# Optimization experiments

Hardware: AMD Instinct MI355X
Metric: run time of the kernel (lower is better)

The kernel has to match this reference:

```python
import jax, jax.numpy as jnp
import numpy as np

EPS = 1e-6
DIM_HEAD = 32
INP = 128
OUP = 128
IH = IW = 32


def _conv3x3(x, w):
    # NCHW conv, 3x3, stride 1, pad 1, no bias
    return jax.lax.conv_general_dilated(
        x, w, window_strides=(1, 1), padding=((1, 1), (1, 1)),
        dimension_numbers=("NCHW", "OIHW", "NCHW"))


def _groupnorm1(x, gamma, beta):
    # GroupNorm with 1 group: normalize over (C,H,W) per sample
    m = jnp.mean(x, axis=(1, 2, 3), keepdims=True)
    v = jnp.var(x, axis=(1, 2, 3), keepdims=True)
    xn = (x - m) * jax.lax.rsqrt(v + EPS)
    return xn * gamma[None, :, None, None] + beta[None, :, None, None]


def _proj(x, w, gamma, beta):
    return jax.nn.gelu(_groupnorm1(_conv3x3(x, w), gamma, beta), approximate=False)


def _relative_index(ih, iw):
    coords = np.stack(np.meshgrid(np.arange(ih), np.arange(iw), indexing="ij"))
    coords = coords.reshape(2, -1)  # (2, N)
    rel = coords[:, :, None] - coords[:, None, :]  # (2, N, N)
    rel[0] += ih - 1
    rel[1] += iw - 1
    rel[0] *= 2 * iw - 1
    return rel.sum(0).reshape(-1).astype(np.int32)  # (N*N,)


def setup_inputs() -> dict:
    key = jax.random.key(0)
    ks = jax.random.split(key, 12)
    B = 16
    x = jax.random.normal(ks[0], (B, INP, IH, IW), jnp.float32)
    w_scale = 0.05
    wq = jax.random.normal(ks[1], (INP, INP, 3, 3), jnp.float32) * w_scale
    wk = jax.random.normal(ks[2], (INP, INP, 3, 3), jnp.float32) * w_scale
    wv = jax.random.normal(ks[3], (INP, INP, 3, 3), jnp.float32) * w_scale
    gq = jnp.ones((INP,), jnp.float32); bq = jnp.zeros((INP,), jnp.float32)
    gk = jnp.ones((INP,), jnp.float32); bk = jnp.zeros((INP,), jnp.float32)
    gv = jnp.ones((INP,), jnp.float32); bv = jnp.zeros((INP,), jnp.float32)
    heads = INP // DIM_HEAD
    table = jax.random.normal(ks[4], ((2 * IH - 1) * (2 * IW - 1), heads), jnp.float32) * 0.02
    rel_index = jnp.asarray(_relative_index(IH, IW))
    out_w = jax.random.normal(ks[5], (OUP, INP, 1, 1), jnp.float32) * w_scale
    out_b = jnp.zeros((OUP,), jnp.float32)
    return {"x": x, "wq": wq, "gq": gq, "bq": bq, "wk": wk, "gk": gk, "bk": bk,
            "wv": wv, "gv": gv, "bv": bv, "table": table, "rel_index": rel_index,
            "out_w": out_w, "out_b": out_b}


def reference(x, wq, gq, bq, wk, gk, bk, wv, gv, bv, table, rel_index, out_w, out_b):
    B, C, ih, iw = x.shape
    H = C // DIM_HEAD
    N = ih * iw

    def to_heads(t):
        # b c ih iw -> b (ihiw) c -> b h n d (heads-major channel split)
        return t.reshape(B, C, N).transpose(0, 2, 1).reshape(B, N, H, DIM_HEAD).transpose(0, 2, 1, 3)

    q = to_heads(_proj(x, wq, gq, bq))
    k = to_heads(_proj(x, wk, gk, bk))
    v = to_heads(_proj(x, wv, gv, bv))

    # NOTE: original applies self.scale only when y is not None; y=None here -> no scale
    dots = jnp.einsum("bhnd,bhmd->bhnm", q, k)  # (B,H,N,N)

    bias = table[rel_index]                 # (N*N, H)
    bias = bias.reshape(N, N, H).transpose(2, 0, 1)[None]  # (1,H,N,N)
    attn = jax.nn.softmax(dots + bias, axis=-1)

    out = jnp.einsum("bhnm,bhmd->bhnd", attn, v)
    out = out.transpose(0, 2, 1, 3).reshape(B, N, C).transpose(0, 2, 1).reshape(B, C, ih, iw)
    # to_out: 1x1 conv + bias (Dropout2d is identity in eval)
    out = jax.lax.conv_general_dilated(
        out, out_w, window_strides=(1, 1), padding=((0, 0), (0, 0)),
        dimension_numbers=("NCHW", "OIHW", "NCHW")) + out_b[None, :, None, None]
    return out
```

## Files before the change

### kernel.cpp

```cpp
#include <hip/hip_runtime.h>

typedef unsigned short u16;
typedef unsigned int   u32;

#define NB   16
#define NC   128
#define NPIX 1024
#define NH   4
#define DH   32

typedef __attribute__((ext_vector_type(8))) short short8;
typedef __attribute__((ext_vector_type(4))) float f32x4;
typedef __attribute__((ext_vector_type(8))) _Float16 half8;

#define XROWS 1152

__device__ __forceinline__ float bf2f(u16 u) {
    return __uint_as_float(((u32)u) << 16);
}
__device__ __forceinline__ u16 f2bf(float f) {
    u32 u = __float_as_uint(f);
    u32 r = (u + 0x7fffu + ((u >> 16) & 1u)) >> 16;
    return (u16)r;
}
__device__ __forceinline__ u16 f2h(float f) {
    _Float16 h = (_Float16)f;
    u16 r; __builtin_memcpy(&r, &h, 2); return r;
}
__device__ __forceinline__ int pk_h2(float a, float b) {
    auto h = __builtin_amdgcn_cvt_pkrtz(a, b);
    int r; __builtin_memcpy(&r, &h, 4); return r;
}
__device__ __forceinline__ float loadf(const void* p, int i, int isf) {
    return isf ? ((const float*)p)[i] : bf2f(((const u16*)p)[i]);
}
__device__ __forceinline__ float4 load4(const void* p, int i4, int isf) {
    if (isf) return ((const float4*)p)[i4];
    ushort4 u = ((const ushort4*)p)[i4];
    return make_float4(bf2f(u.x), bf2f(u.y), bf2f(u.z), bf2f(u.w));
}
__device__ __forceinline__ int detect_isf(const void* x) {
    const u16* p = (const u16*)x;
    u16 v = p[threadIdx.x & 63];
    int e = (v >> 7) & 0xFF;
    unsigned long long m = __ballot(e >= 134);
    return m != 0ull ? 1 : 0;
}

__global__ __launch_bounds__(256) void prep_all(
        const void* __restrict__ x,
        const void* __restrict__ w0, const void* __restrict__ w1,
        const void* __restrict__ w2, const void* __restrict__ ow,
        const int* __restrict__ rel, const void* __restrict__ table,
        u16* __restrict__ Wt, u16* __restrict__ Wf, u16* __restrict__ xTp,
        u16* __restrict__ biasT, float* __restrict__ stats) {
    __shared__ __align__(16) u32 smem_u[4160];
    int isf = detect_isf(x);
    int bid = blockIdx.x;
    int t = threadIdx.x;

    if (bid < 1792) {
        if (bid == 0 && t < 96) stats[t] = 0.f;
        int i = bid * 256 + t;
        if (i < 442368) {
            int j   = i / 147456;
            int rr  = i % 147456;
            int tap = rr >> 14;
            int co  = (rr >> 7) & 127;
            int ci  = rr & 127;
            const void* w = (j == 0) ? w0 : ((j == 1) ? w1 : w2);
            float v = loadf(w, (co * 128 + ci) * 9 + tap, isf);
            Wt[i] = f2bf(v);
        } else {
            int i2 = i - 442368;
            if (i2 < 16384) Wf[i2] = f2h(loadf(ow, i2, isf));
        }
    } else if (bid < 2304) {
        float* tile = (float*)smem_u;
        int b2 = bid - 1792;
        int pixg = b2 & 7, cig = (b2 >> 3) & 3, b = b2 >> 5;

        if (pixg == 0 || pixg == 7) {
            int row = (pixg == 0 ? 0 : 1088) + (t >> 2);
            int seg = t & 3;
            size_t dst = ((size_t)(b * XROWS + row)) * 128 + cig * 32 + seg * 8;
            *(uint4*)&xTp[dst] = make_uint4(0, 0, 0, 0);
        }

        int ci = t >> 3, px0 = (t & 7) * 16;
        int base = b * (NC * NPIX) + (cig * 32 + ci) * NPIX + pixg * 128 + px0;
#pragma unroll
        for (int u = 0; u < 4; ++u) {
            float4 v = load4(x, (base >> 2) + u, isf);
            float* d = &tile[ci * 129 + px0 + u * 4];
            d[0] = v.x; d[1] = v.y; d[2] = v.z; d[3] = v.w;
        }
        __syncthreads();
#pragma unroll
        for (int u = 0; u < 2; ++u) {
            int c = t + u * 256;
            int pix = c >> 2, seg = c & 3;
            u16 tmp[8];
#pragma unroll
            for (int e = 0; e < 8; ++e)
                tmp[e] = f2bf(tile[(seg * 8 + e) * 129 + pix]);
            size_t dst = ((size_t)(b * XROWS + 64 + pixg * 128 + pix)) * 128
                       + cig * 32 + seg * 8;
            *(ushort4*)&xTp[dst] =
                make_ushort4(tmp[0], tmp[1], tmp[2], tmp[3]);
            *(ushort4*)&xTp[dst + 4] =
                make_ushort4(tmp[4], tmp[5], tmp[6], tmp[7]);
        }
    } else {
        int* rl = (int*)smem_u;
        int b2 = bid - 2304;
        int nt = b2 & 15, mt = b2 >> 4;

#pragma unroll
        for (int c = 0; c < 16; ++c) {
            int i = t + c * 256;
            int r = i >> 6, cc = i & 63;
            rl[r * 65 + cc] = rel[(size_t)(nt * 64 + r) * 1024 + mt * 64 + cc];
        }
        __syncthreads();

#pragma unroll
        for (int h = 0; h < NH; ++h) {
#pragma unroll
            for (int c = 0; c < 16; ++c) {
                int wdx = t + c * 256;
                int m = wdx >> 6, n = wdx & 63;
                int ri = rl[n * 65 + m];
                float v = loadf(table, ri * NH + h, isf);
                biasT[((size_t)h << 20) + (size_t)(mt * 64 + m) * 1024
                      + nt * 64 + n] = f2bf(v);
            }
        }
    }
}

__global__ __launch_bounds__(256) void conv6_kernel(
        const u16* __restrict__ xTp, const u16* __restrict__ Wt,
        float* __restrict__ conv_out, float* __restrict__ stats) {
    __shared__ __align__(16) u16 Xh[194 * 128];

    int t = threadIdx.x;
    int pt = blockIdx.x, b = blockIdx.y, j = blockIdx.z;
    int p0 = pt * 128;
    int w = t >> 6, lane = t & 63;
    int q = lane >> 4, l16 = lane & 15;
    int cobase = (w & 1) * 64;
    int pixbase = (w >> 1) * 64;

    const u16* xb  = xTp + ((size_t)b * XROWS + 64) * 128;
    const u16* wjb = Wt + (size_t)j * 9 * 16384;

#pragma unroll
    for (int k = 0; k < 13; ++k) {
        int c = t + k * 256;
        if (c < 194 * 16) {
            int row = c >> 4, seg = c & 15;
            int pg = p0 - 33 + row;
            uint4 v = *(const uint4*)(xb + (size_t)pg * 128 + seg * 8);
            *(uint4*)&Xh[row * 128 + ((seg + row) & 15) * 8] = v;
        }
    }
    __syncthreads();

    f32x4 acc[4][4];
#pragma unroll
    for (int mt = 0; mt < 4; ++mt)
#pragma unroll
        for (int nt = 0; nt < 4; ++nt) acc[mt][nt] = (f32x4)0.f;

    for (int tap = 0; tap < 9; ++tap) {
        int dy = tap / 3, dx = tap % 3;
        bool inv_e = (dx == 0) && (l16 == 0);
        bool inv_o = (dx == 2) && (l16 == 15);
        int rbase = pixbase + dy * 32 + dx + l16;
        const u16* wt = wjb + tap * 16384;
#pragma unroll
        for (int ks = 0; ks < 4; ++ks) {
            int k0 = ks * 32 + q * 8;
            int sl = ks * 4 + q;
            short8 a[4], bf[4];
#pragma unroll
            for (int mt = 0; mt < 4; ++mt)
                a[mt] = *(const short8*)(wt
                        + (size_t)(cobase + mt * 16 + l16) * 128 + k0);
#pragma unroll
            for (int nt = 0; nt < 4; ++nt) {
                int row = rbase + nt * 16;
                short8 v = *(const short8*)&Xh[row * 128
                                               + ((sl + row) & 15) * 8];
                bf[nt] = ((nt & 1) ? inv_o : inv_e) ? (short8)0 : v;
            }
#pragma unroll
            for (int mt = 0; mt < 4; ++mt)
#pragma unroll
                for (int nt = 0; nt < 4; ++nt)
                    acc[mt][nt] = __builtin_amdgcn_mfma_f32_16x16x32_bf16(
                        a[mt], bf[nt], acc[mt][nt], 0, 0, 0);
        }
    }

    float s = 0.f, s2 = 0.f;
    size_t obase = ((size_t)(j * NB + b) * NC) * NPIX;
#pragma unroll
    for (int mt = 0; mt < 4; ++mt) {
#pragma unroll
        for (int nt = 0; nt < 4; ++nt) {
            f32x4 v = acc[mt][nt];
            int co  = cobase + mt * 16 + q * 4;
            int pix = p0 + pixbase + nt * 16 + l16;
#pragma unroll
            for (int r = 0; r < 4; ++r) {
                float val = v[r];
                conv_out[obase + (size_t)(co + r) * NPIX + pix] = val;
                s += val;
                s2 = fmaf(val, val, s2);
            }
        }
    }
#pragma unroll
    for (int off = 32; off; off >>= 1) {
        s  += __shfl_down(s,  (unsigned)off, 64);
        s2 += __shfl_down(s2, (unsigned)off, 64);
    }
    if (lane == 0) {
        atomicAdd(&stats[(j * NB + b) * 2 + 0], s);
        atomicAdd(&stats[(j * NB + b) * 2 + 1], s2);
    }
}

__global__ __launch_bounds__(256) void norm_kernel(
        const void* __restrict__ xdet,
        const float* __restrict__ conv_out, const float* __restrict__ stats,
        const void* __restrict__ g0, const void* __restrict__ b0,
        const void* __restrict__ g1, const void* __restrict__ b1,
        const void* __restrict__ g2, const void* __restrict__ b2,
        u16* __restrict__ qh, u16* __restrict__ kh, u16* __restrict__ vh) {
    __shared__ float tile[32 * 257];
    int isf = detect_isf(xdet);
    int t = threadIdx.x;
    int n0 = blockIdx.x * 256;
    int h = blockIdx.y;
    int z = blockIdx.z;
    int j = z >> 4;
    int b = z & 15;
    const void* gam = (j == 0) ? g0 : ((j == 1) ? g1 : g2);
    const void* bet = (j == 0) ? b0 : ((j == 1) ? b1 : b2);

    float sum = stats[z * 2], ss = stats[z * 2 + 1];
    const float inv = 1.0f / 131072.0f;
    float mean = sum * inv;
    float var  = fmaxf(ss * inv - mean * mean, 0.f);
    float rstd = rsqrtf(var + 1e-6f);

    const float* src = conv_out + ((size_t)z * NC + h * DH) * NPIX + n0;

    if (j == 2) {
        u16* dst = vh + (((size_t)(b * NH + h)) * DH) * NPIX + n0;
#pragma unroll
        for (int cl = 0; cl < 32; ++cl) {
            float v = src[cl * NPIX + t];
            v = (v - mean) * rstd * loadf(gam, h * DH + cl, isf)
              + loadf(bet, h * DH + cl, isf);
            v = 0.5f * v * (1.0f + erff(v * 0.70710678118654752f));
            dst[(size_t)cl * NPIX + t] = f2h(v);
        }
        return;
    }

#pragma unroll
    for (int cl = 0; cl < 32; ++cl) tile[cl * 257 + t] = src[cl * NPIX + t];
    __syncthreads();

    u16* dst = ((j == 0) ? qh : kh)
             + (((size_t)(b * NH + h)) * NPIX + n0) * DH;
#pragma unroll
    for (int k = 0; k < 32; ++k) {
        int o = t + k * 256;
        int d = o & 31, nl = o >> 5;
        float v = tile[d * 257 + nl];
        v = (v - mean) * rstd * loadf(gam, h * DH + d, isf)
          + loadf(bet, h * DH + d, isf);
        v = 0.5f * v * (1.0f + erff(v * 0.70710678118654752f));
        dst[o] = f2h(v);
    }
}

__global__ __launch_bounds__(256) void attn2_kernel(
        const u16* __restrict__ qh, const u16* __restrict__ kh,
        const u16* __restrict__ vh, const u16* __restrict__ biasT,
        u16* __restrict__ attfh) {
    int t = threadIdx.x;
    int b = blockIdx.x, h = blockIdx.y, qt = blockIdx.z;
    int w = t >> 6, lane = t & 63, q = lane >> 4, l16 = lane & 15;
    int nrow0 = qt * 128 + w * 32;

    const u16* qb = qh + (((size_t)(b * NH + h)) * NPIX) * DH;
    const u16* kb = kh + (((size_t)(b * NH + h)) * NPIX) * DH;
    const u16* vb = vh + (((size_t)(b * NH + h)) * DH) * NPIX;
    const u16* bb = biasT + ((size_t)h << 20);

    half8 qf[2];
#pragma unroll
    for (int nt = 0; nt < 2; ++nt)
        qf[nt] = *(const half8*)(qb + (size_t)(nrow0 + nt * 16 + l16) * DH
                                 + q * 8);

    f32x4 O[2][2];
#pragma unroll
    for (int dt = 0; dt < 2; ++dt)
#pragma unroll
        for (int nt = 0; nt < 2; ++nt) O[dt][nt] = (f32x4)0.f;
    float mrow[2] = {-1e30f, -1e30f}, lrow[2] = {0.f, 0.f};

    int addrLo = ((2 * (q & 1)) * 16 + l16) * 4;
    int addrHi = addrLo + 64;
    bool hiQ = (q >= 2);

    for (int kc = 0; kc < 8; ++kc) {
        int m0 = kc * 128;
        f32x4 St[8][2];
#pragma unroll
        for (int mt = 0; mt < 8; ++mt) {
            half8 kf = *(const half8*)(kb + (size_t)(m0 + mt * 16 + l16) * DH
                                       + q * 8);
            St[mt][0] = __builtin_amdgcn_mfma_f32_16x16x32_f16(
                kf, qf[0], (f32x4)0.f, 0, 0, 0);
            St[mt][1] = __builtin_amdgcn_mfma_f32_16x16x32_f16(
                kf, qf[1], (f32x4)0.f, 0, 0, 0);
        }
        float mx[2] = {-1e30f, -1e30f};
#pragma unroll
        for (int mt = 0; mt < 8; ++mt)
#pragma unroll
            for (int nt = 0; nt < 2; ++nt) {
                const u16* bp = bb + (size_t)(m0 + mt * 16 + q * 4) * 1024
                              + nrow0 + nt * 16 + l16;
#pragma unroll
                for (int r = 0; r < 4; ++r) {
                    float v = St[mt][nt][r] + bf2f(bp[(size_t)r * 1024]);
                    St[mt][nt][r] = v;
                    mx[nt] = fmaxf(mx[nt], v);
                }
            }
        float alpha[2];
#pragma unroll
        for (int nt = 0; nt < 2; ++nt) {
            mx[nt] = fmaxf(mx[nt], __shfl_xor(mx[nt], 16, 64));
            mx[nt] = fmaxf(mx[nt], __shfl_xor(mx[nt], 32, 64));
            float mn = fmaxf(mrow[nt], mx[nt]);
            alpha[nt] = __expf(mrow[nt] - mn);
            mrow[nt] = mn;
        }
        float sm[2] = {0.f, 0.f};
#pragma unroll
        for (int mt = 0; mt < 8; ++mt)
#pragma unroll
            for (int nt = 0; nt < 2; ++nt)
#pragma unroll
                for (int r = 0; r < 4; ++r) {
                    float p = __expf(St[mt][nt][r] - mrow[nt]);
                    St[mt][nt][r] = p;
                    sm[nt] += p;
                }
#pragma unroll
        for (int nt = 0; nt < 2; ++nt) {
            sm[nt] += __shfl_xor(sm[nt], 16, 64);
            sm[nt] += __shfl_xor(sm[nt], 32, 64);
            lrow[nt] = lrow[nt] * alpha[nt] + sm[nt];
        }
#pragma unroll
        for (int dt = 0; dt < 2; ++dt)
#pragma unroll
            for (int nt = 0; nt < 2; ++nt)
#pragma unroll
                for (int r = 0; r < 4; ++r)
                    O[dt][nt][r] *= alpha[nt];
#pragma unroll
        for (int ms = 0; ms < 4; ++ms) {
            half8 vf[2];
#pragma unroll
            for (int dt = 0; dt < 2; ++dt)
                vf[dt] = *(const half8*)(vb + (size_t)(dt * 16 + l16) * NPIX
                                         + m0 + ms * 32 + q * 8);
#pragma unroll
            for (int nt = 0; nt < 2; ++nt) {
                int p01_0 = pk_h2(St[2 * ms][nt][0],     St[2 * ms][nt][1]);
                int p23_0 = pk_h2(St[2 * ms][nt][2],     St[2 * ms][nt][3]);
                int p01_1 = pk_h2(St[2 * ms + 1][nt][0], St[2 * ms + 1][nt][1]);
                int p23_1 = pk_h2(St[2 * ms + 1][nt][2], St[2 * ms + 1][nt][3]);
                int a0 = __builtin_amdgcn_ds_bpermute(addrLo, p01_0);
                int a1 = __builtin_amdgcn_ds_bpermute(addrLo, p23_0);
                int a2 = __builtin_amdgcn_ds_bpermute(addrHi, p01_0);
                int a3 = __builtin_amdgcn_ds_bpermute(addrHi, p23_0);
                int b0 = __builtin_amdgcn_ds_bpermute(addrLo, p01_1);
                int b1 = __builtin_amdgcn_ds_bpermute(addrLo, p23_1);
                int b2 = __builtin_amdgcn_ds_bpermute(addrHi, p01_1);
                int b3 = __builtin_amdgcn_ds_bpermute(addrHi, p23_1);
                int pb[4];
                pb[0] = hiQ ? b0 : a0;
                pb[1] = hiQ ? b1 : a1;
                pb[2] = hiQ ? b2 : a2;
                pb[3] = hiQ ? b3 : a3;
                half8 pf; __builtin_memcpy(&pf, pb, 16);
#pragma unroll
                for (int dt = 0; dt < 2; ++dt)
                    O[dt][nt] = __builtin_amdgcn_mfma_f32_16x16x32_f16(
                        vf[dt], pf, O[dt][nt], 0, 0, 0);
            }
        }
    }

#pragma unroll
    for (int nt = 0; nt < 2; ++nt) {
        float rl = 1.0f / lrow[nt];
        int n = nrow0 + nt * 16 + l16;
        u16* dst = attfh + ((size_t)b * NPIX + n) * NC + h * DH;
#pragma unroll
        for (int dt = 0; dt < 2; ++dt) {
            f32x4 o = O[dt][nt];
            uint2 pv = make_uint2((u32)pk_h2(o[0] * rl, o[1] * rl),
                                  (u32)pk_h2(o[2] * rl, o[3] * rl));
            *(uint2*)(dst + dt * 16 + q * 4) = pv;
        }
    }
}

__global__ __launch_bounds__(256) void out3_kernel(
        const void* __restrict__ xdet,
        const u16* __restrict__ attfh, const u16* __restrict__ Wf,
        const void* __restrict__ ob, void* __restrict__ out) {
    int isf = detect_isf(xdet);
    int t = threadIdx.x;
    int n0 = blockIdx.x * 64, b = blockIdx.y;
    int w = t >> 6, lane = t & 63, q = lane >> 4, l16 = lane & 15;
    int cobase = (w & 1) * 64, nbase = (w >> 1) * 32;

    f32x4 acc[4][2];
#pragma unroll
    for (int mt = 0; mt < 4; ++mt)
#pragma unroll
        for (int nt = 0; nt < 2; ++nt) acc[mt][nt] = (f32x4)0.f;

    const u16* ab = attfh + ((size_t)b * NPIX + n0 + nbase) * NC;
#pragma unroll
    for (int ks = 0; ks < 4; ++ks) {
        int k0 = ks * 32 + q * 8;
        half8 a[4], bfr[2];
#pragma unroll
        for (int mt = 0; mt < 4; ++mt)
            a[mt] = *(const half8*)(Wf + (size_t)(cobase + mt * 16 + l16) * NC
                                    + k0);
#pragma unroll
        for (int nt = 0; nt < 2; ++nt)
            bfr[nt] = *(const half8*)(ab + (size_t)(nt * 16 + l16) * NC + k0);
#pragma unroll
        for (int mt = 0; mt < 4; ++mt)
#pragma unroll
            for (int nt = 0; nt < 2; ++nt)
                acc[mt][nt] = __builtin_amdgcn_mfma_f32_16x16x32_f16(
                    a[mt], bfr[nt], acc[mt][nt], 0, 0, 0);
    }

#pragma unroll
    for (int mt = 0; mt < 4; ++mt) {
#pragma unroll
        for (int nt = 0; nt < 2; ++nt) {
            f32x4 v = acc[mt][nt];
            int n = n0 + nbase + nt * 16 + l16;
#pragma unroll
            for (int r = 0; r < 4; ++r) {
                int co = cobase + mt * 16 + q * 4 + r;
                float val = v[r] + loadf(ob, co, isf);
                size_t oidx = ((size_t)b * NC + co) * NPIX + n;
                if (isf) ((float*)out)[oidx] = val;
                else     ((u16*)out)[oidx]   = f2bf(val);
            }
        }
    }
}

extern "C" void kernel_launch(void* const* d_in, const int* in_sizes, int n_in,
                              void* d_out, int out_size, void* d_ws,
                              size_t ws_size, hipStream_t stream) {
    (void)in_sizes; (void)n_in; (void)out_size; (void)ws_size;
    const void* x     = d_in[0];
    const void* wq    = d_in[1];
    const void* gq    = d_in[2];
    const void* bq    = d_in[3];
    const void* wk    = d_in[4];
    const void* gk    = d_in[5];
    const void* bk    = d_in[6];
    const void* wv    = d_in[7];
    const void* gv    = d_in[8];
    const void* bv    = d_in[9];
    const void* table = d_in[10];
    const int*  rel   = (const int*)d_in[11];
    const void* ow    = d_in[12];
    const void* ob    = d_in[13];

    char* ws = (char*)d_ws;
    float* stats = (float*)(ws);
    char*  regQ  = ws + 512;
    u16*   xTp   = (u16*)regQ;
    u16*   Wt    = (u16*)(regQ + 5242880);
    u16*   qhp   = (u16*)regQ;
    u16*   khp   = (u16*)(regQ + 4194304);
    u16*   vhp   = (u16*)(regQ + 8388608);
    u16*   biasT = (u16*)(regQ + 12582912);
    u16*   Wf    = (u16*)(regQ + 20971520);
    char*  regA  = regQ + 25165824;
    float* conv  = (float*)regA;
    u16*   attfh = (u16*)(regA + 8388608);

    prep_all<<<2560, 256, 0, stream>>>(x, wq, wk, wv, ow, rel, table,
                                       Wt, Wf, xTp, biasT, stats);
    conv6_kernel<<<dim3(8, 16, 3), 256, 0, stream>>>(xTp, Wt, conv, stats);
    norm_kernel<<<dim3(4, 4, 48), 256, 0, stream>>>(x, conv, stats,
                                                    gq, bq, gk, bk, gv, bv,
                                                    qhp, khp, vhp);
    attn2_kernel<<<dim3(16, 4, 8), 256, 0, stream>>>(qhp, khp, vhp, biasT,
                                                     attfh);
    out3_kernel<<<dim3(16, 16), 256, 0, stream>>>(x, attfh, Wf, ob, d_out);
}
```

Baseline: 213.9 us.

## Store bias row-major for vector loads; halve conv pixel tile for more blocks

The relative-position bias is now written in natural (n,m) order straight from rel_index, with no shared-memory transpose. The attention kernel then reads four consecutive bias values with one 8-byte load instead of four strided scalar loads. The conv kernel's pixel tile drops from 128 to 64 per block, doubling the grid from 384 to 768 blocks for better occupancy and lowering LDS use. The cost is more redundant weight loads and more halo rows per block.

```diff
diff --git a/kernel.cpp b/kernel.cpp
--- a/kernel.cpp
+++ b/kernel.cpp
@@ -53,7 +53,7 @@
         const void* __restrict__ w2, const void* __restrict__ ow,
         const int* __restrict__ rel, const void* __restrict__ table,
         u16* __restrict__ Wt, u16* __restrict__ Wf, u16* __restrict__ xTp,
-        u16* __restrict__ biasT, float* __restrict__ stats) {
+        u16* __restrict__ biasb, float* __restrict__ stats) {
     __shared__ __align__(16) u32 smem_u[4160];
     int isf = detect_isf(x);
     int bid = blockIdx.x;
@@ -112,53 +112,42 @@
                 make_ushort4(tmp[4], tmp[5], tmp[6], tmp[7]);
         }
     } else {
-        int* rl = (int*)smem_u;
         int b2 = bid - 2304;
         int nt = b2 & 15, mt = b2 >> 4;
-
 #pragma unroll
         for (int c = 0; c < 16; ++c) {
             int i = t + c * 256;
-            int r = i >> 6, cc = i & 63;
-            rl[r * 65 + cc] = rel[(size_t)(nt * 64 + r) * 1024 + mt * 64 + cc];
-        }
-        __syncthreads();
-
-#pragma unroll
-        for (int h = 0; h < NH; ++h) {
-#pragma unroll
-            for (int c = 0; c < 16; ++c) {
-                int wdx = t + c * 256;
-                int m = wdx >> 6, n = wdx & 63;
-                int ri = rl[n * 65 + m];
-                float v = loadf(table, ri * NH + h, isf);
-                biasT[((size_t)h << 20) + (size_t)(mt * 64 + m) * 1024
-                      + nt * 64 + n] = f2bf(v);
-            }
-        }
-    }
-}
-
-__global__ __launch_bounds__(256) void conv6_kernel(
+            int n = i >> 6, m = i & 63;
+            size_t nm = (size_t)(nt * 64 + n) * 1024 + mt * 64 + m;
+            int ri = rel[nm];
+#pragma unroll
+            for (int h = 0; h < NH; ++h)
+                biasb[((size_t)h << 20) + nm] =
+                    f2bf(loadf(table, ri * NH + h, isf));
+        }
+    }
+}
+
+__global__ __launch_bounds__(256) void conv8_kernel(
         const u16* __restrict__ xTp, const u16* __restrict__ Wt,
         float* __restrict__ conv_out, float* __restrict__ stats) {
-    __shared__ __align__(16) u16 Xh[194 * 128];
+    __shared__ __align__(16) u16 Xh[130 * 128];
 
     int t = threadIdx.x;
     int pt = blockIdx.x, b = blockIdx.y, j = blockIdx.z;
-    int p0 = pt * 128;
+    int p0 = pt * 64;
     int w = t >> 6, lane = t & 63;
     int q = lane >> 4, l16 = lane & 15;
     int cobase = (w & 1) * 64;
-    int pixbase = (w >> 1) * 64;
+    int pixbase = (w >> 1) * 32;
 
     const u16* xb  = xTp + ((size_t)b * XROWS + 64) * 128;
     const u16* wjb = Wt + (size_t)j * 9 * 16384;
 
 #pragma unroll
-    for (int k = 0; k < 13; ++k) {
+    for (int k = 0; k < 9; ++k) {
         int c = t + k * 256;
-        if (c < 194 * 16) {
+        if (c < 130 * 16) {
             int row = c >> 4, seg = c & 15;
             int pg = p0 - 33 + row;
             uint4 v = *(const uint4*)(xb + (size_t)pg * 128 + seg * 8);
@@ -167,11 +156,11 @@
     }
     __syncthreads();
 
-    f32x4 acc[4][4];
+    f32x4 acc[4][2];
 #pragma unroll
     for (int mt = 0; mt < 4; ++mt)
 #pragma unroll
-        for (int nt = 0; nt < 4; ++nt) acc[mt][nt] = (f32x4)0.f;
+        for (int nt = 0; nt < 2; ++nt) acc[mt][nt] = (f32x4)0.f;
 
     for (int tap = 0; tap < 9; ++tap) {
         int dy = tap / 3, dx = tap % 3;
@@ -183,22 +172,22 @@
         for (int ks = 0; ks < 4; ++ks) {
             int k0 = ks * 32 + q * 8;
             int sl = ks * 4 + q;
-            short8 a[4], bf[4];
+            short8 a[4], bf[2];
 #pragma unroll
             for (int mt = 0; mt < 4; ++mt)
                 a[mt] = *(const short8*)(wt
                         + (size_t)(cobase + mt * 16 + l16) * 128 + k0);
 #pragma unroll
-            for (int nt = 0; nt < 4; ++nt) {
+            for (int nt = 0; nt < 2; ++nt) {
                 int row = rbase + nt * 16;
                 short8 v = *(const short8*)&Xh[row * 128
                                                + ((sl + row) & 15) * 8];
-                bf[nt] = ((nt & 1) ? inv_o : inv_e) ? (short8)0 : v;
+                bf[nt] = (nt ? inv_o : inv_e) ? (short8)0 : v;
             }
 #pragma unroll
             for (int mt = 0; mt < 4; ++mt)
 #pragma unroll
-                for (int nt = 0; nt < 4; ++nt)
+                for (int nt = 0; nt < 2; ++nt)
                     acc[mt][nt] = __builtin_amdgcn_mfma_f32_16x16x32_bf16(
                         a[mt], bf[nt], acc[mt][nt], 0, 0, 0);
         }
@@ -209,7 +198,7 @@
 #pragma unroll
     for (int mt = 0; mt < 4; ++mt) {
 #pragma unroll
-        for (int nt = 0; nt < 4; ++nt) {
+        for (int nt = 0; nt < 2; ++nt) {
             f32x4 v = acc[mt][nt];
             int co  = cobase + mt * 16 + q * 4;
             int pix = p0 + pixbase + nt * 16 + l16;
@@ -292,7 +281,7 @@
 
 __global__ __launch_bounds__(256) void attn2_kernel(
         const u16* __restrict__ qh, const u16* __restrict__ kh,
-        const u16* __restrict__ vh, const u16* __restrict__ biasT,
+        const u16* __restrict__ vh, const u16* __restrict__ biasb,
         u16* __restrict__ attfh) {
     int t = threadIdx.x;
     int b = blockIdx.x, h = blockIdx.y, qt = blockIdx.z;
@@ -302,7 +291,7 @@
     const u16* qb = qh + (((size_t)(b * NH + h)) * NPIX) * DH;
     const u16* kb = kh + (((size_t)(b * NH + h)) * NPIX) * DH;
     const u16* vb = vh + (((size_t)(b * NH + h)) * DH) * NPIX;
-    const u16* bb = biasT + ((size_t)h << 20);
+    const u16* bb = biasb + ((size_t)h << 20);
 
     half8 qf[2];
 #pragma unroll
@@ -338,11 +327,13 @@
         for (int mt = 0; mt < 8; ++mt)
 #pragma unroll
             for (int nt = 0; nt < 2; ++nt) {
-                const u16* bp = bb + (size_t)(m0 + mt * 16 + q * 4) * 1024
-                              + nrow0 + nt * 16 + l16;
+                ushort4 u = *(const ushort4*)(bb
+                    + (size_t)(nrow0 + nt * 16 + l16) * 1024
+                    + m0 + mt * 16 + q * 4);
+                u16 ua[4]; __builtin_memcpy(ua, &u, 8);
 #pragma unroll
                 for (int r = 0; r < 4; ++r) {
-                    float v = St[mt][nt][r] + bf2f(bp[(size_t)r * 1024]);
+                    float v = St[mt][nt][r] + bf2f(ua[r]);
                     St[mt][nt][r] = v;
                     mx[nt] = fmaxf(mx[nt], v);
                 }
@@ -511,19 +502,19 @@
     u16*   qhp   = (u16*)regQ;
     u16*   khp   = (u16*)(regQ + 4194304);
     u16*   vhp   = (u16*)(regQ + 8388608);
-    u16*   biasT = (u16*)(regQ + 12582912);
+    u16*   biasb = (u16*)(regQ + 12582912);
     u16*   Wf    = (u16*)(regQ + 20971520);
     char*  regA  = regQ + 25165824;
     float* conv  = (float*)regA;
     u16*   attfh = (u16*)(regA + 8388608);
 
     prep_all<<<2560, 256, 0, stream>>>(x, wq, wk, wv, ow, rel, table,
-                                       Wt, Wf, xTp, biasT, stats);
-    conv6_kernel<<<dim3(8, 16, 3), 256, 0, stream>>>(xTp, Wt, conv, stats);
+                                       Wt, Wf, xTp, biasb, stats);
+    conv8_kernel<<<dim3(16, 16, 3), 256, 0, stream>>>(xTp, Wt, conv, stats);
     norm_kernel<<<dim3(4, 4, 48), 256, 0, stream>>>(x, conv, stats,
                                                     gq, bq, gk, bk, gv, bv,
                                                     qhp, khp, vhp);
-    attn2_kernel<<<dim3(16, 4, 8), 256, 0, stream>>>(qhp, khp, vhp, biasT,
+    attn2_kernel<<<dim3(16, 4, 8), 256, 0, stream>>>(qhp, khp, vhp, biasb,
                                                      attfh);
     out3_kernel<<<dim3(16, 16), 256, 0, stream>>>(x, attfh, Wf, ob, d_out);
 }
```

Result: slower. 266.3 us (+24.5%).
